# Performance work log

Hardware: AMD Instinct MI355X
Metric: run time of the kernel (lower is better)

## Reference

```python
import jax, jax.numpy as jnp
import numpy as np

N = 100_000      # graph nodes
E = 3_200_000    # graph edges == line-graph nodes
NNZ = 6_400_000  # pm_pd nonzeros (~2 per edge)
IN = 16
OUT = 16
BN_EPS = 1e-5


def setup_inputs() -> dict:
    key = jax.random.key(0)
    ks = jax.random.split(key, 16)
    w = lambda k, shp: (jax.random.normal(k, shp, dtype=jnp.float32) * 0.1)
    inp = {
        "feat_a": jax.random.normal(ks[0], (N, IN), dtype=jnp.float32),
        "feat_b": jax.random.normal(ks[1], (E, IN), dtype=jnp.float32),
        "deg": jax.random.uniform(ks[2], (N, 1), dtype=jnp.float32),
        "pm_vals": jnp.ones((NNZ,), dtype=jnp.float32),
        "W_prev": w(ks[3], (IN, OUT)), "b_prev": w(ks[4], (OUT,)),
        "W_deg": w(ks[5], (IN, OUT)), "b_deg": w(ks[6], (OUT,)),
        "W_rad": w(ks[7], (3, IN, OUT)), "b_rad": w(ks[8], (3, OUT)),
        "W_fuse": w(ks[9], (IN, OUT)), "b_fuse": w(ks[10], (OUT,)),
        "bn_gamma": jnp.ones((OUT,), dtype=jnp.float32),
        "bn_beta": jnp.zeros((OUT,), dtype=jnp.float32),
        "src": jax.random.randint(ks[11], (E,), 0, N, dtype=jnp.int32),
        "dst": jax.random.randint(ks[12], (E,), 0, N, dtype=jnp.int32),
        "pm_rows": jax.random.randint(ks[13], (NNZ,), 0, N, dtype=jnp.int32),
        "pm_cols": jax.random.randint(ks[14], (NNZ,), 0, E, dtype=jnp.int32),
        "radius": 3,
    }
    return inp


def _hop(z, src, dst, n):
    # copy_src + sum: new_z[d] = sum_{(s,d) in E} z[s]
    return jax.ops.segment_sum(z[src], dst, num_segments=n)


def reference(feat_a, feat_b, deg, pm_vals, W_prev, b_prev, W_deg, b_deg,
              W_rad, b_rad, W_fuse, b_fuse, bn_gamma, bn_beta,
              src, dst, pm_rows, pm_cols, radius):
    n = feat_a.shape[0]
    prev_proj = feat_a @ W_prev + b_prev
    deg_proj = (deg * feat_a) @ W_deg + b_deg

    # aggregate_radius: hops 1, 2, 4, ..., 2^(radius-1)
    z = _hop(feat_a, src, dst, n)
    z_list = [z]
    for i in range(radius - 1):
        for _ in range(2 ** i):
            z = _hop(z, src, dst, n)
        z_list.append(z)
    radius_proj = sum(zk @ W_rad[k] + b_rad[k] for k, zk in enumerate(z_list))

    # sparse pm_pd @ feat_b via COO gather-scatter
    pm_y = jax.ops.segment_sum(pm_vals[:, None] * feat_b[pm_cols], pm_rows,
                               num_segments=n)
    fuse = pm_y @ W_fuse + b_fuse

    result = prev_proj + deg_proj + radius_proj + fuse
    half = result.shape[1] // 2
    result = jnp.concatenate(
        [result[:, :half], jax.nn.relu(result[:, half:])], axis=1)

    # BatchNorm1d, training mode (batch stats, biased variance)
    mean = jnp.mean(result, axis=0)
    var = jnp.mean((result - mean) ** 2, axis=0)
    return (result - mean) * jax.lax.rsqrt(var + BN_EPS) * bn_gamma + bn_beta
```

## Files before the change

### kernel.cpp

```cpp
#include <hip/hip_runtime.h>
#include <math.h>

#define Nn    100000
#define Ee    3200000
#define NNZn  6400000
#define NF    (Nn * 16)
#define K     256
#define RPB   391
#define CHUNK 16384

__global__ __launch_bounds__(256) void count_kernel(
    const int* __restrict__ keys, int n, int* __restrict__ tot) {
  __shared__ int h[K];
  int t = threadIdx.x;
  if (t < K) h[t] = 0;
  __syncthreads();
  int base = blockIdx.x * CHUNK;
  int end = min(base + CHUNK, n);
  for (int i = base + t; i < end; i += 256) atomicAdd(&h[keys[i] / RPB], 1);
  __syncthreads();
  if (t < K && h[t]) atomicAdd(&tot[t], h[t]);
}

__global__ __launch_bounds__(K) void scan_kernel(
    const int* __restrict__ tot_e, const int* __restrict__ tot_p,
    int* __restrict__ bs_e, int* __restrict__ cur_e,
    int* __restrict__ bs_p, int* __restrict__ cur_p) {
  const int* tot = (blockIdx.x == 0) ? tot_e : tot_p;
  int* bs  = (blockIdx.x == 0) ? bs_e  : bs_p;
  int* cur = (blockIdx.x == 0) ? cur_e : cur_p;
  __shared__ int s[K];
  int t = threadIdx.x;
  s[t] = tot[t];
  __syncthreads();
  for (int off = 1; off < K; off <<= 1) {
    int v = (t >= off) ? s[t - off] : 0;
    __syncthreads();
    s[t] += v;
    __syncthreads();
  }
  int excl = t ? s[t - 1] : 0;
  bs[t] = excl;
  cur[t] = excl;
  if (t == K - 1) bs[K] = s[K - 1];
}

__global__ __launch_bounds__(256) void bin_edges(
    const int* __restrict__ dst, const int* __restrict__ src,
    int* __restrict__ cur, int* __restrict__ binned) {
  __shared__ int h[K];
  int t = threadIdx.x;
  if (t < K) h[t] = 0;
  __syncthreads();
  int base = blockIdx.x * CHUNK;
  int end = min(base + CHUNK, Ee);
  for (int i = base + t; i < end; i += 256) atomicAdd(&h[dst[i] / RPB], 1);
  __syncthreads();
  if (t < K) {
    int c = h[t];
    h[t] = c ? atomicAdd(&cur[t], c) : 0;
  }
  __syncthreads();
  for (int i = base + t; i < end; i += 256) {
    int d = dst[i];
    int k = d / RPB;
    int lr = d - k * RPB;
    int pos = atomicAdd(&h[k], 1);
    binned[pos] = (lr << 17) | src[i];
  }
}

__global__ __launch_bounds__(256) void bin_pm(
    const int* __restrict__ rows, const int* __restrict__ cols,
    const float* __restrict__ vals,
    int* __restrict__ cur, int2* __restrict__ bp) {
  __shared__ int h[K];
  int t = threadIdx.x;
  if (t < K) h[t] = 0;
  __syncthreads();
  int base = blockIdx.x * CHUNK;
  int end = min(base + CHUNK, NNZn);
  for (int i = base + t; i < end; i += 256) atomicAdd(&h[rows[i] / RPB], 1);
  __syncthreads();
  if (t < K) {
    int c = h[t];
    h[t] = c ? atomicAdd(&cur[t], c) : 0;
  }
  __syncthreads();
  for (int i = base + t; i < end; i += 256) {
    int r = rows[i];
    int k = r / RPB;
    int lr = r - k * RPB;
    int pos = atomicAdd(&h[k], 1);
    bp[pos] = make_int2((lr << 22) | cols[i], __float_as_int(vals[i]));
  }
}

__global__ __launch_bounds__(1024) void sort_edges(
    const int* __restrict__ be, const int* __restrict__ bs,
    int* __restrict__ csr, int* __restrict__ rp) {
  __shared__ int hist[RPB];
  __shared__ int sc[512];
  int b = blockIdx.x, t = threadIdx.x;
  if (t < RPB) hist[t] = 0;
  __syncthreads();
  int s0 = bs[b], s1 = bs[b + 1];
  for (int i = s0 + t; i < s1; i += 1024)
    atomicAdd(&hist[be[i] >> 17], 1);
  __syncthreads();
  if (t < 512) sc[t] = (t < RPB) ? hist[t] : 0;
  __syncthreads();
  for (int off = 1; off < 512; off <<= 1) {
    int v = 0;
    if (t < 512 && t >= off) v = sc[t - off];
    __syncthreads();
    if (t < 512) sc[t] += v;
    __syncthreads();
  }
  int r0 = b * RPB;
  if (t < RPB) {
    int r = r0 + t;
    if (r < Nn) rp[r + 1] = s0 + sc[t];
    hist[t] = s0 + sc[t] - hist[t];
  }
  if (b == 0 && t == 0) rp[0] = 0;
  __syncthreads();
  for (int i = s0 + t; i < s1; i += 1024) {
    int p = be[i];
    int pos = atomicAdd(&hist[p >> 17], 1);
    csr[pos] = p & 0x1FFFF;
  }
}

__global__ __launch_bounds__(1024) void sort_pm(
    const int2* __restrict__ bpi, const int* __restrict__ bs, int b0,
    int2* __restrict__ dcsr, int* __restrict__ rp) {
  __shared__ int hist[RPB];
  __shared__ int sc[512];
  int b = b0 + blockIdx.x, t = threadIdx.x;
  if (t < RPB) hist[t] = 0;
  __syncthreads();
  int s0 = bs[b], s1 = bs[b + 1];
  int base = s0 - bs[b0];
  for (int i = s0 + t; i < s1; i += 1024)
    atomicAdd(&hist[bpi[i].x >> 22], 1);
  __syncthreads();
  if (t < 512) sc[t] = (t < RPB) ? hist[t] : 0;
  __syncthreads();
  for (int off = 1; off < 512; off <<= 1) {
    int v = 0;
    if (t < 512 && t >= off) v = sc[t - off];
    __syncthreads();
    if (t < 512) sc[t] += v;
    __syncthreads();
  }
  int r0 = b * RPB;
  if (t < RPB) {
    int r = r0 + t;
    if (r < Nn) rp[r + 1] = base + sc[t];
    hist[t] = base + sc[t] - hist[t];
  }
  if (b == b0 && t == 0) rp[r0] = 0;
  __syncthreads();
  for (int i = s0 + t; i < s1; i += 1024) {
    int2 e = bpi[i];
    int pos = atomicAdd(&hist[e.x >> 22], 1);
    dcsr[pos] = make_int2(e.x & 0x3FFFFF, e.y);
  }
}

__global__ __launch_bounds__(256) void hop_csr4(
    const float* __restrict__ zin, float* __restrict__ zout,
    const int* __restrict__ cs, const int* __restrict__ rp) {
  int gid = (blockIdx.x * 256 + threadIdx.x) >> 2;
  int q = (threadIdx.x & 3) * 4;
  if (gid >= Nn) return;
  int j = rp[gid], e = rp[gid + 1];
  float ax = 0.f, ay = 0.f, az = 0.f, aw = 0.f;
  for (; j + 8 <= e; j += 8) {
    int s0 = cs[j],     s1 = cs[j + 1], s2 = cs[j + 2], s3 = cs[j + 3];
    int s4 = cs[j + 4], s5 = cs[j + 5], s6 = cs[j + 6], s7 = cs[j + 7];
    float4 x0 = *(const float4*)(zin + (size_t)s0 * 16 + q);
    float4 x1 = *(const float4*)(zin + (size_t)s1 * 16 + q);
    float4 x2 = *(const float4*)(zin + (size_t)s2 * 16 + q);
    float4 x3 = *(const float4*)(zin + (size_t)s3 * 16 + q);
    float4 x4 = *(const float4*)(zin + (size_t)s4 * 16 + q);
    float4 x5 = *(const float4*)(zin + (size_t)s5 * 16 + q);
    float4 x6 = *(const float4*)(zin + (size_t)s6 * 16 + q);
    float4 x7 = *(const float4*)(zin + (size_t)s7 * 16 + q);
    ax += ((x0.x + x1.x) + (x2.x + x3.x)) + ((x4.x + x5.x) + (x6.x + x7.x));
    ay += ((x0.y + x1.y) + (x2.y + x3.y)) + ((x4.y + x5.y) + (x6.y + x7.y));
    az += ((x0.z + x1.z) + (x2.z + x3.z)) + ((x4.z + x5.z) + (x6.z + x7.z));
    aw += ((x0.w + x1.w) + (x2.w + x3.w)) + ((x4.w + x5.w) + (x6.w + x7.w));
  }
  for (; j < e; ++j) {
    float4 x = *(const float4*)(zin + (size_t)cs[j] * 16 + q);
    ax += x.x; ay += x.y; az += x.z; aw += x.w;
  }
  *(float4*)(zout + (size_t)gid * 16 + q) = make_float4(ax, ay, az, aw);
}

__global__ __launch_bounds__(256) void pm_csr4(
    const float* __restrict__ fb, const int2* __restrict__ bp,
    const int* __restrict__ rp, float* __restrict__ pmy,
    int r0, int r1) {
  int gid = r0 + ((blockIdx.x * 256 + threadIdx.x) >> 2);
  int q = (threadIdx.x & 3) * 4;
  if (gid >= r1) return;
  int j = rp[gid], e = rp[gid + 1];
  float ax = 0.f, ay = 0.f, az = 0.f, aw = 0.f;
  for (; j + 8 <= e; j += 8) {
    int2 e0 = bp[j];     int2 e1 = bp[j + 1];
    int2 e2 = bp[j + 2]; int2 e3 = bp[j + 3];
    int2 e4 = bp[j + 4]; int2 e5 = bp[j + 5];
    int2 e6 = bp[j + 6]; int2 e7 = bp[j + 7];
    float4 x0 = *(const float4*)(fb + (size_t)e0.x * 16 + q);
    float4 x1 = *(const float4*)(fb + (size_t)e1.x * 16 + q);
    float4 x2 = *(const float4*)(fb + (size_t)e2.x * 16 + q);
    float4 x3 = *(const float4*)(fb + (size_t)e3.x * 16 + q);
    float4 x4 = *(const float4*)(fb + (size_t)e4.x * 16 + q);
    float4 x5 = *(const float4*)(fb + (size_t)e5.x * 16 + q);
    float4 x6 = *(const float4*)(fb + (size_t)e6.x * 16 + q);
    float4 x7 = *(const float4*)(fb + (size_t)e7.x * 16 + q);
    float v0 = __int_as_float(e0.y), v1 = __int_as_float(e1.y);
    float v2 = __int_as_float(e2.y), v3 = __int_as_float(e3.y);
    float v4 = __int_as_float(e4.y), v5 = __int_as_float(e5.y);
    float v6 = __int_as_float(e6.y), v7 = __int_as_float(e7.y);
    ax = fmaf(v0, x0.x, ax); ay = fmaf(v0, x0.y, ay);
    az = fmaf(v0, x0.z, az); aw = fmaf(v0, x0.w, aw);
    ax = fmaf(v1, x1.x, ax); ay = fmaf(v1, x1.y, ay);
    az = fmaf(v1, x1.z, az); aw = fmaf(v1, x1.w, aw);
    ax = fmaf(v2, x2.x, ax); ay = fmaf(v2, x2.y, ay);
    az = fmaf(v2, x2.z, az); aw = fmaf(v2, x2.w, aw);
    ax = fmaf(v3, x3.x, ax); ay = fmaf(v3, x3.y, ay);
    az = fmaf(v3, x3.z, az); aw = fmaf(v3, x3.w, aw);
    ax = fmaf(v4, x4.x, ax); ay = fmaf(v4, x4.y, ay);
    az = fmaf(v4, x4.z, az); aw = fmaf(v4, x4.w, aw);
    ax = fmaf(v5, x5.x, ax); ay = fmaf(v5, x5.y, ay);
    az = fmaf(v5, x5.z, az); aw = fmaf(v5, x5.w, aw);
    ax = fmaf(v6, x6.x, ax); ay = fmaf(v6, x6.y, ay);
    az = fmaf(v6, x6.z, az); aw = fmaf(v6, x6.w, aw);
    ax = fmaf(v7, x7.x, ax); ay = fmaf(v7, x7.y, ay);
    az = fmaf(v7, x7.z, az); aw = fmaf(v7, x7.w, aw);
  }
  for (; j < e; ++j) {
    int2 ee = bp[j];
    float4 x = *(const float4*)(fb + (size_t)ee.x * 16 + q);
    float v = __int_as_float(ee.y);
    ax = fmaf(v, x.x, ax); ay = fmaf(v, x.y, ay);
    az = fmaf(v, x.z, az); aw = fmaf(v, x.w, aw);
  }
  *(float4*)(pmy + (size_t)gid * 16 + q) = make_float4(ax, ay, az, aw);
}

__global__ __launch_bounds__(256) void fuse_kernel(
    const float* __restrict__ feat_a, const float* __restrict__ deg,
    const float* __restrict__ z1, const float* __restrict__ z2,
    const float* __restrict__ z4, const float* __restrict__ pmy,
    const float* __restrict__ Wprev, const float* __restrict__ bprev,
    const float* __restrict__ Wdeg,  const float* __restrict__ bdeg,
    const float* __restrict__ Wrad,  const float* __restrict__ brad,
    const float* __restrict__ Wfuse, const float* __restrict__ bfuse,
    float* __restrict__ result, float* __restrict__ stats) {
  __shared__ float sWp[256], sWd[256], sWr[768], sWf[256], sB[16];
  __shared__ float sstat[32];
  int t = threadIdx.x;
  sWp[t] = Wprev[t];
  sWd[t] = Wdeg[t];
  sWf[t] = Wfuse[t];
  for (int i = t; i < 768; i += 256) sWr[i] = Wrad[i];
  if (t < 32) sstat[t] = 0.f;
  if (t < 16)
    sB[t] = bprev[t] + bdeg[t] + brad[t] + brad[16 + t] + brad[32 + t] + bfuse[t];
  __syncthreads();

  int n = blockIdx.x * 256 + t;
  bool valid = n < Nn;
  int nc = valid ? n : (Nn - 1);

  float dg = deg[nc];
  float out[16];
#pragma unroll
  for (int o = 0; o < 16; ++o) out[o] = sB[o];

  const float4* pa = (const float4*)(feat_a + (size_t)nc * 16);
  const float4* p1 = (const float4*)(z1 + (size_t)nc * 16);
  const float4* p2 = (const float4*)(z2 + (size_t)nc * 16);
  const float4* p4 = (const float4*)(z4 + (size_t)nc * 16);
  const float4* pp = (const float4*)(pmy + (size_t)nc * 16);

#define FUSE_STEP(E, XA, X1, X2, X4, XP)                                  \
  {                                                                       \
    int i = c * 4 + (E);                                                  \
    float va = (XA);                                                      \
    float vd = dg * va;                                                   \
    float v1 = (X1), v2 = (X2), v4 = (X4), vp = (XP);                     \
    _Pragma("unroll")                                                     \
    for (int o = 0; o < 16; ++o) {                                        \
      float acc = out[o];                                                 \
      acc = fmaf(va, sWp[i * 16 + o], acc);                               \
      acc = fmaf(vd, sWd[i * 16 + o], acc);                               \
      acc = fmaf(v1, sWr[i * 16 + o], acc);                               \
      acc = fmaf(v2, sWr[256 + i * 16 + o], acc);                         \
      acc = fmaf(v4, sWr[512 + i * 16 + o], acc);                         \
      acc = fmaf(vp, sWf[i * 16 + o], acc);                               \
      out[o] = acc;                                                       \
    }                                                                     \
  }

#pragma unroll
  for (int c = 0; c < 4; ++c) {
    float4 xa = pa[c];
    float4 x1 = p1[c];
    float4 x2 = p2[c];
    float4 x4 = p4[c];
    float4 xp = pp[c];
    FUSE_STEP(0, xa.x, x1.x, x2.x, x4.x, xp.x)
    FUSE_STEP(1, xa.y, x1.y, x2.y, x4.y, xp.y)
    FUSE_STEP(2, xa.z, x1.z, x2.z, x4.z, xp.z)
    FUSE_STEP(3, xa.w, x1.w, x2.w, x4.w, xp.w)
  }
#undef FUSE_STEP

#pragma unroll
  for (int o = 8; o < 16; ++o) out[o] = fmaxf(out[o], 0.f);

  if (valid) {
    float4* r = (float4*)(result + (size_t)n * 16);
    r[0] = make_float4(out[0], out[1], out[2], out[3]);
    r[1] = make_float4(out[4], out[5], out[6], out[7]);
    r[2] = make_float4(out[8], out[9], out[10], out[11]);
    r[3] = make_float4(out[12], out[13], out[14], out[15]);
  } else {
#pragma unroll
    for (int o = 0; o < 16; ++o) out[o] = 0.f;
  }

#pragma unroll
  for (int o = 0; o < 16; ++o) {
    float s = out[o];
    float qq = out[o] * out[o];
#pragma unroll
    for (int m = 32; m >= 1; m >>= 1) {
      s += __shfl_xor(s, m, 64);
      qq += __shfl_xor(qq, m, 64);
    }
    if ((t & 63) == 0) {
      atomicAdd(&sstat[o], s);
      atomicAdd(&sstat[16 + o], qq);
    }
  }
  __syncthreads();
  if (t < 32) atomicAdd(&stats[t], sstat[t]);
}

__global__ void bn_coeffs(float* __restrict__ stats,
                          const float* __restrict__ gamma,
                          const float* __restrict__ beta) {
  int t = threadIdx.x;
  if (t < 16) {
    float mean = stats[t] * (1.0f / Nn);
    float var  = stats[16 + t] * (1.0f / Nn) - mean * mean;
    float sc   = gamma[t] * rsqrtf(var + 1e-5f);
    stats[32 + t] = sc;
    stats[48 + t] = beta[t] - mean * sc;
  }
}

__global__ __launch_bounds__(256) void bn_apply(
    float* __restrict__ result, const float* __restrict__ stats) {
  int idx = blockIdx.x * 256 + threadIdx.x;
  if (idx >= Nn * 4) return;
  int c = (idx & 3) * 4;
  float4 r = ((const float4*)result)[idx];
  float4 o;
  o.x = r.x * stats[32 + c + 0] + stats[48 + c + 0];
  o.y = r.y * stats[32 + c + 1] + stats[48 + c + 1];
  o.z = r.z * stats[32 + c + 2] + stats[48 + c + 2];
  o.w = r.w * stats[32 + c + 3] + stats[48 + c + 3];
  ((float4*)result)[idx] = o;
}

extern "C" void kernel_launch(void* const* d_in, const int* in_sizes, int n_in,
                              void* d_out, int out_size, void* d_ws, size_t ws_size,
                              hipStream_t stream) {
  const float* feat_a  = (const float*)d_in[0];
  const float* feat_b  = (const float*)d_in[1];
  const float* deg     = (const float*)d_in[2];
  const float* pm_vals = (const float*)d_in[3];
  const float* W_prev  = (const float*)d_in[4];
  const float* b_prev  = (const float*)d_in[5];
  const float* W_deg   = (const float*)d_in[6];
  const float* b_deg   = (const float*)d_in[7];
  const float* W_rad   = (const float*)d_in[8];
  const float* b_rad   = (const float*)d_in[9];
  const float* W_fuse  = (const float*)d_in[10];
  const float* b_fuse  = (const float*)d_in[11];
  const float* bn_g    = (const float*)d_in[12];
  const float* bn_b    = (const float*)d_in[13];
  const int*   src     = (const int*)d_in[14];
  const int*   dst     = (const int*)d_in[15];
  const int*   pm_rows = (const int*)d_in[16];
  const int*   pm_cols = (const int*)d_in[17];

  int* ws = (int*)d_ws;
  int*   A    = ws;
  int*   B    = ws + (size_t)Ee;
  float* pm_y = (float*)(ws + (size_t)Ee + 2 * (size_t)NNZn);
  int*   T    = (int*)(pm_y + NF);
  int*   tot_e = T;
  int*   tot_p = T + K;
  float* stats = (float*)(T + 2 * K);
  int*   bs_e  = T + 2 * K + 64;
  int*   cur_e = bs_e + K + 1;
  int*   bs_p  = cur_e + K;
  int*   cur_p = bs_p + K + 1;
  int*   rp_e  = cur_p + K;
  int*   rp_p  = rp_e + Nn + 1;

  int2*  bp       = (int2*)B;
  int2*  dcsr     = (int2*)A;
  int*   binned_e = B;
  int*   csr_src  = A;
  float* z1 = (float*)B;
  float* z2 = z1 + (size_t)NF;
  float* z3 = z2 + (size_t)NF;
  float* z4 = z3 + (size_t)NF;
  float* result = (float*)d_out;

  hipMemsetAsync(T, 0, (size_t)(2 * K + 64) * sizeof(int), stream);

  int cb_e = (Ee + CHUNK - 1) / CHUNK;
  int cb_p = (NNZn + CHUNK - 1) / CHUNK;
  count_kernel<<<cb_e, 256, 0, stream>>>(dst, Ee, tot_e);
  count_kernel<<<cb_p, 256, 0, stream>>>(pm_rows, NNZn, tot_p);
  scan_kernel<<<2, K, 0, stream>>>(tot_e, tot_p, bs_e, cur_e, bs_p, cur_p);

  bin_pm<<<cb_p, 256, 0, stream>>>(pm_rows, pm_cols, pm_vals, cur_p, bp);
  const int pb[6] = {0, 52, 103, 154, 205, 256};
  for (int q = 0; q < 5; ++q) {
    int b0 = pb[q], b1 = pb[q + 1];
    sort_pm<<<b1 - b0, 1024, 0, stream>>>(bp, bs_p, b0, dcsr, rp_p);
    int r0 = b0 * RPB;
    int r1 = (b1 * RPB < Nn) ? b1 * RPB : Nn;
    int nb = ((r1 - r0) * 4 + 255) / 256;
    pm_csr4<<<nb, 256, 0, stream>>>(feat_b, dcsr, rp_p, pm_y, r0, r1);
  }

  bin_edges<<<cb_e, 256, 0, stream>>>(dst, src, cur_e, binned_e);
  sort_edges<<<K, 1024, 0, stream>>>(binned_e, bs_e, csr_src, rp_e);

  int hop_blocks = (Nn * 4 + 255) / 256;
  hop_csr4<<<hop_blocks, 256, 0, stream>>>(feat_a, z1, csr_src, rp_e);
  hop_csr4<<<hop_blocks, 256, 0, stream>>>(z1, z2, csr_src, rp_e);
  hop_csr4<<<hop_blocks, 256, 0, stream>>>(z2, z3, csr_src, rp_e);
  hop_csr4<<<hop_blocks, 256, 0, stream>>>(z3, z4, csr_src, rp_e);

  int fuse_blocks = (Nn + 255) / 256;
  fuse_kernel<<<fuse_blocks, 256, 0, stream>>>(
      feat_a, deg, z1, z2, z4, pm_y,
      W_prev, b_prev, W_deg, b_deg, W_rad, b_rad, W_fuse, b_fuse,
      result, stats);

  bn_coeffs<<<1, 64, 0, stream>>>(stats, bn_g, bn_b);

  int bn_blocks = (Nn * 4 + 255) / 256;
  bn_apply<<<bn_blocks, 256, 0, stream>>>(result, stats);
}
```

Before: 1.136 ms.

## Replace pm sort+CSR SpMM with per-bin shared-memory atomic accumulation; vectorize binning loads

The pm_pd product no longer sorts each row bucket into CSR and then runs a separate gather kernel. A single kernel now walks each bucket's binned entries, gathers the full 16-float feat_b row, and accumulates into a padded shared-memory tile of 391 rows using LDS float atomics before writing pm_y. Separately, the count and binning kernels load keys, cols and vals as int4/float4 to cut load instructions. This removes a global scatter pass and several launches, but adds many LDS atomics that can contend. Float summation order also becomes nondeterministic.

```diff
diff --git a/kernel.cpp b/kernel.cpp
--- a/kernel.cpp
+++ b/kernel.cpp
@@ -17,7 +17,13 @@
   __syncthreads();
   int base = blockIdx.x * CHUNK;
   int end = min(base + CHUNK, n);
-  for (int i = base + t; i < end; i += 256) atomicAdd(&h[keys[i] / RPB], 1);
+  for (int i = base + t * 4; i < end; i += 1024) {
+    int4 k4 = *(const int4*)(keys + i);
+    atomicAdd(&h[k4.x / RPB], 1);
+    atomicAdd(&h[k4.y / RPB], 1);
+    atomicAdd(&h[k4.z / RPB], 1);
+    atomicAdd(&h[k4.w / RPB], 1);
+  }
   __syncthreads();
   if (t < K && h[t]) atomicAdd(&tot[t], h[t]);
 }
@@ -54,19 +60,34 @@
   __syncthreads();
   int base = blockIdx.x * CHUNK;
   int end = min(base + CHUNK, Ee);
-  for (int i = base + t; i < end; i += 256) atomicAdd(&h[dst[i] / RPB], 1);
+  for (int i = base + t * 4; i < end; i += 1024) {
+    int4 d4 = *(const int4*)(dst + i);
+    atomicAdd(&h[d4.x / RPB], 1);
+    atomicAdd(&h[d4.y / RPB], 1);
+    atomicAdd(&h[d4.z / RPB], 1);
+    atomicAdd(&h[d4.w / RPB], 1);
+  }
   __syncthreads();
   if (t < K) {
     int c = h[t];
     h[t] = c ? atomicAdd(&cur[t], c) : 0;
   }
   __syncthreads();
-  for (int i = base + t; i < end; i += 256) {
-    int d = dst[i];
-    int k = d / RPB;
-    int lr = d - k * RPB;
-    int pos = atomicAdd(&h[k], 1);
-    binned[pos] = (lr << 17) | src[i];
+  for (int i = base + t * 4; i < end; i += 1024) {
+    int4 d4 = *(const int4*)(dst + i);
+    int4 s4 = *(const int4*)(src + i);
+#define BE_ONE(D, S)                                    \
+    {                                                   \
+      int k = (D) / RPB;                                \
+      int lr = (D) - k * RPB;                           \
+      int pos = atomicAdd(&h[k], 1);                    \
+      binned[pos] = (lr << 17) | (S);                   \
+    }
+    BE_ONE(d4.x, s4.x)
+    BE_ONE(d4.y, s4.y)
+    BE_ONE(d4.z, s4.z)
+    BE_ONE(d4.w, s4.w)
+#undef BE_ONE
   }
 }
 
@@ -80,20 +101,95 @@
   __syncthreads();
   int base = blockIdx.x * CHUNK;
   int end = min(base + CHUNK, NNZn);
-  for (int i = base + t; i < end; i += 256) atomicAdd(&h[rows[i] / RPB], 1);
+  for (int i = base + t * 4; i < end; i += 1024) {
+    int4 r4 = *(const int4*)(rows + i);
+    atomicAdd(&h[r4.x / RPB], 1);
+    atomicAdd(&h[r4.y / RPB], 1);
+    atomicAdd(&h[r4.z / RPB], 1);
+    atomicAdd(&h[r4.w / RPB], 1);
+  }
   __syncthreads();
   if (t < K) {
     int c = h[t];
     h[t] = c ? atomicAdd(&cur[t], c) : 0;
   }
   __syncthreads();
-  for (int i = base + t; i < end; i += 256) {
-    int r = rows[i];
-    int k = r / RPB;
-    int lr = r - k * RPB;
-    int pos = atomicAdd(&h[k], 1);
-    bp[pos] = make_int2((lr << 22) | cols[i], __float_as_int(vals[i]));
-  }
+  for (int i = base + t * 4; i < end; i += 1024) {
+    int4 r4 = *(const int4*)(rows + i);
+    int4 c4 = *(const int4*)(cols + i);
+    float4 v4 = *(const float4*)(vals + i);
+#define BP_ONE(R, C, V)                                         \
+    {                                                           \
+      int k = (R) / RPB;                                        \
+      int lr = (R) - k * RPB;                                   \
+      int pos = atomicAdd(&h[k], 1);                            \
+      bp[pos] = make_int2((lr << 22) | (C), __float_as_int(V)); \
+    }
+    BP_ONE(r4.x, c4.x, v4.x)
+    BP_ONE(r4.y, c4.y, v4.y)
+    BP_ONE(r4.z, c4.z, v4.z)
+    BP_ONE(r4.w, c4.w, v4.w)
+#undef BP_ONE
+  }
+}
+
+__global__ __launch_bounds__(1024) void pm_fused(
+    const float* __restrict__ fb, const int2* __restrict__ bp,
+    const int* __restrict__ bs, float* __restrict__ pmy) {
+  __shared__ float acc[RPB * 17];
+  int b = blockIdx.x, t = threadIdx.x;
+  for (int i = t; i < RPB * 17; i += 1024) acc[i] = 0.f;
+  __syncthreads();
+  int s0 = bs[b], s1 = bs[b + 1];
+  int i = s0 + t;
+  for (; i + 1024 < s1; i += 2048) {
+    int2 e0 = bp[i];
+    int2 e1 = bp[i + 1024];
+    const float4* p0 = (const float4*)(fb + (size_t)(e0.x & 0x3FFFFF) * 16);
+    const float4* p1 = (const float4*)(fb + (size_t)(e1.x & 0x3FFFFF) * 16);
+    float4 a0 = p0[0], b0 = p0[1], c0 = p0[2], d0 = p0[3];
+    float4 a1 = p1[0], b1 = p1[1], c1 = p1[2], d1 = p1[3];
+    float v0 = __int_as_float(e0.y);
+    float v1 = __int_as_float(e1.y);
+    float* q0 = &acc[(e0.x >> 22) * 17];
+    float* q1 = &acc[(e1.x >> 22) * 17];
+    atomicAdd(&q0[0],  v0 * a0.x); atomicAdd(&q0[1],  v0 * a0.y);
+    atomicAdd(&q0[2],  v0 * a0.z); atomicAdd(&q0[3],  v0 * a0.w);
+    atomicAdd(&q0[4],  v0 * b0.x); atomicAdd(&q0[5],  v0 * b0.y);
+    atomicAdd(&q0[6],  v0 * b0.z); atomicAdd(&q0[7],  v0 * b0.w);
+    atomicAdd(&q0[8],  v0 * c0.x); atomicAdd(&q0[9],  v0 * c0.y);
+    atomicAdd(&q0[10], v0 * c0.z); atomicAdd(&q0[11], v0 * c0.w);
+    atomicAdd(&q0[12], v0 * d0.x); atomicAdd(&q0[13], v0 * d0.y);
+    atomicAdd(&q0[14], v0 * d0.z); atomicAdd(&q0[15], v0 * d0.w);
+    atomicAdd(&q1[0],  v1 * a1.x); atomicAdd(&q1[1],  v1 * a1.y);
+    atomicAdd(&q1[2],  v1 * a1.z); atomicAdd(&q1[3],  v1 * a1.w);
+    atomicAdd(&q1[4],  v1 * b1.x); atomicAdd(&q1[5],  v1 * b1.y);
+    atomicAdd(&q1[6],  v1 * b1.z); atomicAdd(&q1[7],  v1 * b1.w);
+    atomicAdd(&q1[8],  v1 * c1.x); atomicAdd(&q1[9],  v1 * c1.y);
+    atomicAdd(&q1[10], v1 * c1.z); atomicAdd(&q1[11], v1 * c1.w);
+    atomicAdd(&q1[12], v1 * d1.x); atomicAdd(&q1[13], v1 * d1.y);
+    atomicAdd(&q1[14], v1 * d1.z); atomicAdd(&q1[15], v1 * d1.w);
+  }
+  for (; i < s1; i += 1024) {
+    int2 e0 = bp[i];
+    const float4* p0 = (const float4*)(fb + (size_t)(e0.x & 0x3FFFFF) * 16);
+    float4 a0 = p0[0], b0 = p0[1], c0 = p0[2], d0 = p0[3];
+    float v0 = __int_as_float(e0.y);
+    float* q0 = &acc[(e0.x >> 22) * 17];
+    atomicAdd(&q0[0],  v0 * a0.x); atomicAdd(&q0[1],  v0 * a0.y);
+    atomicAdd(&q0[2],  v0 * a0.z); atomicAdd(&q0[3],  v0 * a0.w);
+    atomicAdd(&q0[4],  v0 * b0.x); atomicAdd(&q0[5],  v0 * b0.y);
+    atomicAdd(&q0[6],  v0 * b0.z); atomicAdd(&q0[7],  v0 * b0.w);
+    atomicAdd(&q0[8],  v0 * c0.x); atomicAdd(&q0[9],  v0 * c0.y);
+    atomicAdd(&q0[10], v0 * c0.z); atomicAdd(&q0[11], v0 * c0.w);
+    atomicAdd(&q0[12], v0 * d0.x); atomicAdd(&q0[13], v0 * d0.y);
+    atomicAdd(&q0[14], v0 * d0.z); atomicAdd(&q0[15], v0 * d0.w);
+  }
+  __syncthreads();
+  int r0 = b * RPB;
+  int nr = min(RPB, Nn - r0);
+  for (int j = t; j < nr * 16; j += 1024)
+    pmy[(size_t)r0 * 16 + j] = acc[(j >> 4) * 17 + (j & 15)];
 }
 
 __global__ __launch_bounds__(1024) void sort_edges(
@@ -129,43 +225,6 @@
     int p = be[i];
     int pos = atomicAdd(&hist[p >> 17], 1);
     csr[pos] = p & 0x1FFFF;
-  }
-}
-
-__global__ __launch_bounds__(1024) void sort_pm(
-    const int2* __restrict__ bpi, const int* __restrict__ bs, int b0,
-    int2* __restrict__ dcsr, int* __restrict__ rp) {
-  __shared__ int hist[RPB];
-  __shared__ int sc[512];
-  int b = b0 + blockIdx.x, t = threadIdx.x;
-  if (t < RPB) hist[t] = 0;
-  __syncthreads();
-  int s0 = bs[b], s1 = bs[b + 1];
-  int base = s0 - bs[b0];
-  for (int i = s0 + t; i < s1; i += 1024)
-    atomicAdd(&hist[bpi[i].x >> 22], 1);
-  __syncthreads();
-  if (t < 512) sc[t] = (t < RPB) ? hist[t] : 0;
-  __syncthreads();
-  for (int off = 1; off < 512; off <<= 1) {
-    int v = 0;
-    if (t < 512 && t >= off) v = sc[t - off];
-    __syncthreads();
-    if (t < 512) sc[t] += v;
-    __syncthreads();
-  }
-  int r0 = b * RPB;
-  if (t < RPB) {
-    int r = r0 + t;
-    if (r < Nn) rp[r + 1] = base + sc[t];
-    hist[t] = base + sc[t] - hist[t];
-  }
-  if (b == b0 && t == 0) rp[r0] = 0;
-  __syncthreads();
-  for (int i = s0 + t; i < s1; i += 1024) {
-    int2 e = bpi[i];
-    int pos = atomicAdd(&hist[e.x >> 22], 1);
-    dcsr[pos] = make_int2(e.x & 0x3FFFFF, e.y);
   }
 }
 
@@ -200,59 +259,6 @@
   *(float4*)(zout + (size_t)gid * 16 + q) = make_float4(ax, ay, az, aw);
 }
 
-__global__ __launch_bounds__(256) void pm_csr4(
-    const float* __restrict__ fb, const int2* __restrict__ bp,
-    const int* __restrict__ rp, float* __restrict__ pmy,
-    int r0, int r1) {
-  int gid = r0 + ((blockIdx.x * 256 + threadIdx.x) >> 2);
-  int q = (threadIdx.x & 3) * 4;
-  if (gid >= r1) return;
-  int j = rp[gid], e = rp[gid + 1];
-  float ax = 0.f, ay = 0.f, az = 0.f, aw = 0.f;
-  for (; j + 8 <= e; j += 8) {
-    int2 e0 = bp[j];     int2 e1 = bp[j + 1];
-    int2 e2 = bp[j + 2]; int2 e3 = bp[j + 3];
-    int2 e4 = bp[j + 4]; int2 e5 = bp[j + 5];
-    int2 e6 = bp[j + 6]; int2 e7 = bp[j + 7];
-    float4 x0 = *(const float4*)(fb + (size_t)e0.x * 16 + q);
-    float4 x1 = *(const float4*)(fb + (size_t)e1.x * 16 + q);
-    float4 x2 = *(const float4*)(fb + (size_t)e2.x * 16 + q);
-    float4 x3 = *(const float4*)(fb + (size_t)e3.x * 16 + q);
-    float4 x4 = *(const float4*)(fb + (size_t)e4.x * 16 + q);
-    float4 x5 = *(const float4*)(fb + (size_t)e5.x * 16 + q);
-    float4 x6 = *(const float4*)(fb + (size_t)e6.x * 16 + q);
-    float4 x7 = *(const float4*)(fb + (size_t)e7.x * 16 + q);
-    float v0 = __int_as_float(e0.y), v1 = __int_as_float(e1.y);
-    float v2 = __int_as_float(e2.y), v3 = __int_as_float(e3.y);
-    float v4 = __int_as_float(e4.y), v5 = __int_as_float(e5.y);
-    float v6 = __int_as_float(e6.y), v7 = __int_as_float(e7.y);
-    ax = fmaf(v0, x0.x, ax); ay = fmaf(v0, x0.y, ay);
-    az = fmaf(v0, x0.z, az); aw = fmaf(v0, x0.w, aw);
-    ax = fmaf(v1, x1.x, ax); ay = fmaf(v1, x1.y, ay);
-    az = fmaf(v1, x1.z, az); aw = fmaf(v1, x1.w, aw);
-    ax = fmaf(v2, x2.x, ax); ay = fmaf(v2, x2.y, ay);
-    az = fmaf(v2, x2.z, az); aw = fmaf(v2, x2.w, aw);
-    ax = fmaf(v3, x3.x, ax); ay = fmaf(v3, x3.y, ay);
-    az = fmaf(v3, x3.z, az); aw = fmaf(v3, x3.w, aw);
-    ax = fmaf(v4, x4.x, ax); ay = fmaf(v4, x4.y, ay);
-    az = fmaf(v4, x4.z, az); aw = fmaf(v4, x4.w, aw);
-    ax = fmaf(v5, x5.x, ax); ay = fmaf(v5, x5.y, ay);
-    az = fmaf(v5, x5.z, az); aw = fmaf(v5, x5.w, aw);
-    ax = fmaf(v6, x6.x, ax); ay = fmaf(v6, x6.y, ay);
-    az = fmaf(v6, x6.z, az); aw = fmaf(v6, x6.w, aw);
-    ax = fmaf(v7, x7.x, ax); ay = fmaf(v7, x7.y, ay);
-    az = fmaf(v7, x7.z, az); aw = fmaf(v7, x7.w, aw);
-  }
-  for (; j < e; ++j) {
-    int2 ee = bp[j];
-    float4 x = *(const float4*)(fb + (size_t)ee.x * 16 + q);
-    float v = __int_as_float(ee.y);
-    ax = fmaf(v, x.x, ax); ay = fmaf(v, x.y, ay);
-    az = fmaf(v, x.z, az); aw = fmaf(v, x.w, aw);
-  }
-  *(float4*)(pmy + (size_t)gid * 16 + q) = make_float4(ax, ay, az, aw);
-}
-
 __global__ __launch_bounds__(256) void fuse_kernel(
     const float* __restrict__ feat_a, const float* __restrict__ deg,
     const float* __restrict__ z1, const float* __restrict__ z2,
@@ -416,10 +422,8 @@
   int*   bs_p  = cur_e + K;
   int*   cur_p = bs_p + K + 1;
   int*   rp_e  = cur_p + K;
-  int*   rp_p  = rp_e + Nn + 1;
 
   int2*  bp       = (int2*)B;
-  int2*  dcsr     = (int2*)A;
   int*   binned_e = B;
   int*   csr_src  = A;
   float* z1 = (float*)B;
@@ -437,15 +441,7 @@
   scan_kernel<<<2, K, 0, stream>>>(tot_e, tot_p, bs_e, cur_e, bs_p, cur_p);
 
   bin_pm<<<cb_p, 256, 0, stream>>>(pm_rows, pm_cols, pm_vals, cur_p, bp);
-  const int pb[6] = {0, 52, 103, 154, 205, 256};
-  for (int q = 0; q < 5; ++q) {
-    int b0 = pb[q], b1 = pb[q + 1];
-    sort_pm<<<b1 - b0, 1024, 0, stream>>>(bp, bs_p, b0, dcsr, rp_p);
-    int r0 = b0 * RPB;
-    int r1 = (b1 * RPB < Nn) ? b1 * RPB : Nn;
-    int nb = ((r1 - r0) * 4 + 255) / 256;
-    pm_csr4<<<nb, 256, 0, stream>>>(feat_b, dcsr, rp_p, pm_y, r0, r1);
-  }
+  pm_fused<<<K, 1024, 0, stream>>>(feat_b, bp, bs_p, pm_y);
 
   bin_edges<<<cb_e, 256, 0, stream>>>(dst, src, cur_e, binned_e);
   sort_edges<<<K, 1024, 0, stream>>>(binned_e, bs_e, csr_src, rp_e);
```

New measurement: 1.194 ms. 5.1% more time.
